# Performance work log

Measured on AMD Instinct MI355X. Metric: run time of the kernel, lower is better.

Reference implementation:

```python
import jax, jax.numpy as jnp
import numpy as np

R, N1, N2, D = 4, 4096, 4096, 8


def setup_inputs() -> dict:
    key = jax.random.key(0)
    k1, k2, k3 = jax.random.split(key, 3)
    x1 = jax.random.normal(k1, (R, N1, D), dtype=jnp.float32)
    x2 = jax.random.normal(k2, (R, N2, D), dtype=jnp.float32)
    # learned parameters (init: ones), matching nn.Parameter(torch.ones(...))
    lengthscales = jnp.ones((D, 1), dtype=jnp.float32)
    output_scale = jnp.ones((1,), dtype=jnp.float32)
    return {"x1": x1, "x2": x2, "lengthscales": lengthscales, "output_scale": output_scale}


def reference(x1, x2, lengthscales, output_scale):
    # RBF.K: output_scale^2 * exp(-0.5 * sum_d ((x1 - x2) / lengthscales)^2)
    # Computed via the Gram identity ||a-b||^2 = ||a||^2 + ||b||^2 - 2 a.b
    inv_ls = 1.0 / lengthscales.reshape(-1)          # [D]
    a = x1 * inv_ls                                  # [R, N1, D]
    b = x2 * inv_ls                                  # [R, N2, D]
    aa = jnp.sum(a * a, axis=-1)                     # [R, N1]
    bb = jnp.sum(b * b, axis=-1)                     # [R, N2]
    ab = jnp.einsum('rnd,rmd->rnm', a, b)            # [R, N1, N2]
    sqdist = jnp.maximum(aa[:, :, None] + bb[:, None, :] - 2.0 * ab, 0.0)
    return (output_scale[0] ** 2) * jnp.exp(-0.5 * sqdist)
```

## Files before the change

kernel.cpp:

```cpp
#include <hip/hip_runtime.h>


constexpr int D  = 8;
constexpr int BI = 16;
constexpr int BJ = 256;

#if __has_builtin(__builtin_amdgcn_exp2f)
#define FAST_EXP2(x) __builtin_amdgcn_exp2f(x)
#else
#define FAST_EXP2(x) __expf((x) * 0.69314718f)
#endif

__global__ __launch_bounds__(256, 6) void rbf_kernel(
    const float* __restrict__ x1, const float* __restrict__ x2,
    const float* __restrict__ ls, const float* __restrict__ osc,
    float* __restrict__ out, int N1, int N2)
{
    __shared__ float sb[D][BJ];
    __shared__ float sbb[BJ];
    __shared__ float sa[BI][D];
    __shared__ float sasq[BI];

    const int r   = blockIdx.z;
    const int i0  = blockIdx.y * BI;
    const int j0  = blockIdx.x * BJ;
    const int tid = threadIdx.x;

    float4 l0 = *reinterpret_cast<const float4*>(ls);
    float4 l1 = *reinterpret_cast<const float4*>(ls + 4);
    float4 inv0, inv1;
    inv0.x = 1.0f / l0.x; inv0.y = 1.0f / l0.y; inv0.z = 1.0f / l0.z; inv0.w = 1.0f / l0.w;
    inv1.x = 1.0f / l1.x; inv1.y = 1.0f / l1.y; inv1.z = 1.0f / l1.z; inv1.w = 1.0f / l1.w;

    {
        const float* src = x2 + ((size_t)r * N2 + j0 + tid) * D;
        float4 v0 = *reinterpret_cast<const float4*>(src);
        float4 v1 = *reinterpret_cast<const float4*>(src + 4);
        v0.x *= inv0.x; v0.y *= inv0.y; v0.z *= inv0.z; v0.w *= inv0.w;
        v1.x *= inv1.x; v1.y *= inv1.y; v1.z *= inv1.z; v1.w *= inv1.w;
        sb[0][tid] = v0.x; sb[1][tid] = v0.y; sb[2][tid] = v0.z; sb[3][tid] = v0.w;
        sb[4][tid] = v1.x; sb[5][tid] = v1.y; sb[6][tid] = v1.z; sb[7][tid] = v1.w;
        sbb[tid] = v0.x*v0.x + v0.y*v0.y + v0.z*v0.z + v0.w*v0.w
                 + v1.x*v1.x + v1.y*v1.y + v1.z*v1.z + v1.w*v1.w;
    }
    if (tid < BI) {
        const float* src = x1 + ((size_t)r * N1 + i0 + tid) * D;
        float4 v0 = *reinterpret_cast<const float4*>(src);
        float4 v1 = *reinterpret_cast<const float4*>(src + 4);
        v0.x *= inv0.x; v0.y *= inv0.y; v0.z *= inv0.z; v0.w *= inv0.w;
        v1.x *= inv1.x; v1.y *= inv1.y; v1.z *= inv1.z; v1.w *= inv1.w;
        *reinterpret_cast<float4*>(&sa[tid][0]) = v0;
        *reinterpret_cast<float4*>(&sa[tid][4]) = v1;
        sasq[tid] = v0.x*v0.x + v0.y*v0.y + v0.z*v0.z + v0.w*v0.w
                  + v1.x*v1.x + v1.y*v1.y + v1.z*v1.z + v1.w*v1.w;
    }
    const float os2 = osc[0] * osc[0];
    __syncthreads();

    const int lane = tid & 63;
    const int wv   = tid >> 6;

    float4 bd[D];
#pragma unroll
    for (int d = 0; d < D; ++d)
        bd[d] = *reinterpret_cast<const float4*>(&sb[d][lane * 4]);
    const float4 bb4 = *reinterpret_cast<const float4*>(&sbb[lane * 4]);

    constexpr float L2E  = 1.44269504f;
    constexpr float NH2E = -0.72134752f;

    float* obase = out + ((size_t)r * N1 + i0) * (size_t)N2 + j0 + lane * 4;

#pragma unroll
    for (int ii = 0; ii < 4; ++ii) {
        const int row = wv * 4 + ii;
        const float4 a0  = *reinterpret_cast<const float4*>(&sa[row][0]);
        const float4 a1  = *reinterpret_cast<const float4*>(&sa[row][4]);
        const float  asq = sasq[row];

        float4 ch;
        ch.x = (asq + bb4.x) * NH2E;
        ch.y = (asq + bb4.y) * NH2E;
        ch.z = (asq + bb4.z) * NH2E;
        ch.w = (asq + bb4.w) * NH2E;

        float d0 = 0.f, d1 = 0.f, d2 = 0.f, d3 = 0.f;
        const float a[D] = {a0.x, a0.y, a0.z, a0.w, a1.x, a1.y, a1.z, a1.w};
#pragma unroll
        for (int d = 0; d < D; ++d) {
            const float av = a[d];
            d0 = fmaf(av, bd[d].x, d0);
            d1 = fmaf(av, bd[d].y, d1);
            d2 = fmaf(av, bd[d].z, d2);
            d3 = fmaf(av, bd[d].w, d3);
        }
        float4 o;
        o.x = os2 * FAST_EXP2(fmaf(d0, L2E, ch.x));
        o.y = os2 * FAST_EXP2(fmaf(d1, L2E, ch.y));
        o.z = os2 * FAST_EXP2(fmaf(d2, L2E, ch.z));
        o.w = os2 * FAST_EXP2(fmaf(d3, L2E, ch.w));
        *reinterpret_cast<float4*>(obase + (size_t)row * N2) = o;
    }
}

extern "C" void kernel_launch(void* const* d_in, const int* in_sizes, int n_in,
                              void* d_out, int out_size, void* d_ws, size_t ws_size,
                              hipStream_t stream) {
    (void)in_sizes; (void)n_in; (void)d_ws; (void)ws_size; (void)out_size;
    const float* x1  = (const float*)d_in[0];
    const float* x2  = (const float*)d_in[1];
    const float* ls  = (const float*)d_in[2];
    const float* osc = (const float*)d_in[3];
    float* out = (float*)d_out;

    const int R = 4, N1 = 4096, N2 = 4096;
    dim3 grid(N2 / BJ, N1 / BI, R);
    rbf_kernel<<<grid, dim3(256), 0, stream>>>(x1, x2, ls, osc, out, N1, N2);
}
```

Baseline: 51.04 us.

## Enlarge row tile per block and fold output scale into exp argument

Each block now covers 128 rows of x1 instead of 16, with every wave looping over 32 rows and reusing its register-held x2 tile. This cuts the number of blocks and the repeated x2 loads and scaling setup per block. The output scale squared is folded into the exponent as log2, which removes a multiply per element. The occupancy hint is raised to 8. The log2 fold returns NaN or zero for a zero output scale, and the partial unroll of 4 may affect scheduling.

```diff
diff --git a/kernel.cpp b/kernel.cpp
--- a/kernel.cpp
+++ b/kernel.cpp
@@ -1,9 +1,9 @@
 #include <hip/hip_runtime.h>
 
 
-constexpr int D  = 8;
-constexpr int BI = 16;
-constexpr int BJ = 256;
+constexpr int D     = 8;
+constexpr int BROWS = 128;
+constexpr int BJ    = 256;
 
 #if __has_builtin(__builtin_amdgcn_exp2f)
 #define FAST_EXP2(x) __builtin_amdgcn_exp2f(x)
@@ -11,50 +11,55 @@
 #define FAST_EXP2(x) __expf((x) * 0.69314718f)
 #endif
 
-__global__ __launch_bounds__(256, 6) void rbf_kernel(
+__global__ __launch_bounds__(256, 8) void rbf_kernel(
     const float* __restrict__ x1, const float* __restrict__ x2,
     const float* __restrict__ ls, const float* __restrict__ osc,
     float* __restrict__ out, int N1, int N2)
 {
     __shared__ float sb[D][BJ];
     __shared__ float sbb[BJ];
-    __shared__ float sa[BI][D];
-    __shared__ float sasq[BI];
+    __shared__ float sa[BROWS][D];
+    __shared__ float sca[BROWS];
 
     const int r   = blockIdx.z;
-    const int i0  = blockIdx.y * BI;
+    const int i0  = blockIdx.y * BROWS;
     const int j0  = blockIdx.x * BJ;
     const int tid = threadIdx.x;
 
-    float4 l0 = *reinterpret_cast<const float4*>(ls);
-    float4 l1 = *reinterpret_cast<const float4*>(ls + 4);
-    float4 inv0, inv1;
-    inv0.x = 1.0f / l0.x; inv0.y = 1.0f / l0.y; inv0.z = 1.0f / l0.z; inv0.w = 1.0f / l0.w;
-    inv1.x = 1.0f / l1.x; inv1.y = 1.0f / l1.y; inv1.z = 1.0f / l1.z; inv1.w = 1.0f / l1.w;
+    constexpr float L2E  = 1.44269504f;
+    constexpr float NH2E = -0.72134752f;
 
     {
-        const float* src = x2 + ((size_t)r * N2 + j0 + tid) * D;
-        float4 v0 = *reinterpret_cast<const float4*>(src);
-        float4 v1 = *reinterpret_cast<const float4*>(src + 4);
-        v0.x *= inv0.x; v0.y *= inv0.y; v0.z *= inv0.z; v0.w *= inv0.w;
-        v1.x *= inv1.x; v1.y *= inv1.y; v1.z *= inv1.z; v1.w *= inv1.w;
-        sb[0][tid] = v0.x; sb[1][tid] = v0.y; sb[2][tid] = v0.z; sb[3][tid] = v0.w;
-        sb[4][tid] = v1.x; sb[5][tid] = v1.y; sb[6][tid] = v1.z; sb[7][tid] = v1.w;
-        sbb[tid] = v0.x*v0.x + v0.y*v0.y + v0.z*v0.z + v0.w*v0.w
-                 + v1.x*v1.x + v1.y*v1.y + v1.z*v1.z + v1.w*v1.w;
+        float4 l0 = *reinterpret_cast<const float4*>(ls);
+        float4 l1 = *reinterpret_cast<const float4*>(ls + 4);
+        float4 inv0, inv1;
+        inv0.x = 1.0f/l0.x; inv0.y = 1.0f/l0.y; inv0.z = 1.0f/l0.z; inv0.w = 1.0f/l0.w;
+        inv1.x = 1.0f/l1.x; inv1.y = 1.0f/l1.y; inv1.z = 1.0f/l1.z; inv1.w = 1.0f/l1.w;
+
+        {
+            const float* src = x2 + ((size_t)r * N2 + j0 + tid) * D;
+            float4 v0 = *reinterpret_cast<const float4*>(src);
+            float4 v1 = *reinterpret_cast<const float4*>(src + 4);
+            v0.x *= inv0.x; v0.y *= inv0.y; v0.z *= inv0.z; v0.w *= inv0.w;
+            v1.x *= inv1.x; v1.y *= inv1.y; v1.z *= inv1.z; v1.w *= inv1.w;
+            sb[0][tid] = v0.x; sb[1][tid] = v0.y; sb[2][tid] = v0.z; sb[3][tid] = v0.w;
+            sb[4][tid] = v1.x; sb[5][tid] = v1.y; sb[6][tid] = v1.z; sb[7][tid] = v1.w;
+            sbb[tid] = v0.x*v0.x + v0.y*v0.y + v0.z*v0.z + v0.w*v0.w
+                     + v1.x*v1.x + v1.y*v1.y + v1.z*v1.z + v1.w*v1.w;
+        }
+        if (tid < BROWS) {
+            const float* src = x1 + ((size_t)r * N1 + i0 + tid) * D;
+            float4 v0 = *reinterpret_cast<const float4*>(src);
+            float4 v1 = *reinterpret_cast<const float4*>(src + 4);
+            v0.x *= inv0.x; v0.y *= inv0.y; v0.z *= inv0.z; v0.w *= inv0.w;
+            v1.x *= inv1.x; v1.y *= inv1.y; v1.z *= inv1.z; v1.w *= inv1.w;
+            *reinterpret_cast<float4*>(&sa[tid][0]) = v0;
+            *reinterpret_cast<float4*>(&sa[tid][4]) = v1;
+            sca[tid] = (v0.x*v0.x + v0.y*v0.y + v0.z*v0.z + v0.w*v0.w
+                      + v1.x*v1.x + v1.y*v1.y + v1.z*v1.z + v1.w*v1.w) * NH2E;
+        }
     }
-    if (tid < BI) {
-        const float* src = x1 + ((size_t)r * N1 + i0 + tid) * D;
-        float4 v0 = *reinterpret_cast<const float4*>(src);
-        float4 v1 = *reinterpret_cast<const float4*>(src + 4);
-        v0.x *= inv0.x; v0.y *= inv0.y; v0.z *= inv0.z; v0.w *= inv0.w;
-        v1.x *= inv1.x; v1.y *= inv1.y; v1.z *= inv1.z; v1.w *= inv1.w;
-        *reinterpret_cast<float4*>(&sa[tid][0]) = v0;
-        *reinterpret_cast<float4*>(&sa[tid][4]) = v1;
-        sasq[tid] = v0.x*v0.x + v0.y*v0.y + v0.z*v0.z + v0.w*v0.w
-                  + v1.x*v1.x + v1.y*v1.y + v1.z*v1.z + v1.w*v1.w;
-    }
-    const float os2 = osc[0] * osc[0];
+    const float lg2os = __log2f(osc[0] * osc[0]);
     __syncthreads();
 
     const int lane = tid & 63;
@@ -64,42 +69,38 @@
 #pragma unroll
     for (int d = 0; d < D; ++d)
         bd[d] = *reinterpret_cast<const float4*>(&sb[d][lane * 4]);
-    const float4 bb4 = *reinterpret_cast<const float4*>(&sbb[lane * 4]);
+    float4 cb;
+    {
+        const float4 bb = *reinterpret_cast<const float4*>(&sbb[lane * 4]);
+        cb.x = fmaf(bb.x, NH2E, lg2os); cb.y = fmaf(bb.y, NH2E, lg2os);
+        cb.z = fmaf(bb.z, NH2E, lg2os); cb.w = fmaf(bb.w, NH2E, lg2os);
+    }
 
-    constexpr float L2E  = 1.44269504f;
-    constexpr float NH2E = -0.72134752f;
+    float* obase = out + ((size_t)r * N1 + i0 + wv * 32) * (size_t)N2 + j0 + lane * 4;
 
-    float* obase = out + ((size_t)r * N1 + i0) * (size_t)N2 + j0 + lane * 4;
+#pragma unroll 4
+    for (int ii = 0; ii < 32; ++ii) {
+        const int row = wv * 32 + ii;
+        const float4 a0 = *reinterpret_cast<const float4*>(&sa[row][0]);
+        const float4 a1 = *reinterpret_cast<const float4*>(&sa[row][4]);
+        const float  ca = sca[row];
 
-#pragma unroll
-    for (int ii = 0; ii < 4; ++ii) {
-        const int row = wv * 4 + ii;
-        const float4 a0  = *reinterpret_cast<const float4*>(&sa[row][0]);
-        const float4 a1  = *reinterpret_cast<const float4*>(&sa[row][4]);
-        const float  asq = sasq[row];
-
-        float4 ch;
-        ch.x = (asq + bb4.x) * NH2E;
-        ch.y = (asq + bb4.y) * NH2E;
-        ch.z = (asq + bb4.z) * NH2E;
-        ch.w = (asq + bb4.w) * NH2E;
-
-        float d0 = 0.f, d1 = 0.f, d2 = 0.f, d3 = 0.f;
+        float p0 = 0.f, p1 = 0.f, p2 = 0.f, p3 = 0.f;
         const float a[D] = {a0.x, a0.y, a0.z, a0.w, a1.x, a1.y, a1.z, a1.w};
 #pragma unroll
         for (int d = 0; d < D; ++d) {
             const float av = a[d];
-            d0 = fmaf(av, bd[d].x, d0);
-            d1 = fmaf(av, bd[d].y, d1);
-            d2 = fmaf(av, bd[d].z, d2);
-            d3 = fmaf(av, bd[d].w, d3);
+            p0 = fmaf(av, bd[d].x, p0);
+            p1 = fmaf(av, bd[d].y, p1);
+            p2 = fmaf(av, bd[d].z, p2);
+            p3 = fmaf(av, bd[d].w, p3);
         }
         float4 o;
-        o.x = os2 * FAST_EXP2(fmaf(d0, L2E, ch.x));
-        o.y = os2 * FAST_EXP2(fmaf(d1, L2E, ch.y));
-        o.z = os2 * FAST_EXP2(fmaf(d2, L2E, ch.z));
-        o.w = os2 * FAST_EXP2(fmaf(d3, L2E, ch.w));
-        *reinterpret_cast<float4*>(obase + (size_t)row * N2) = o;
+        o.x = FAST_EXP2(fmaf(p0, L2E, ca + cb.x));
+        o.y = FAST_EXP2(fmaf(p1, L2E, ca + cb.y));
+        o.z = FAST_EXP2(fmaf(p2, L2E, ca + cb.z));
+        o.w = FAST_EXP2(fmaf(p3, L2E, ca + cb.w));
+        *reinterpret_cast<float4*>(obase + (size_t)ii * N2) = o;
     }
 }
 
@@ -114,6 +115,6 @@
     float* out = (float*)d_out;
 
     const int R = 4, N1 = 4096, N2 = 4096;
-    dim3 grid(N2 / BJ, N1 / BI, R);
+    dim3 grid(N2 / BJ, N1 / BROWS, R);
     rbf_kernel<<<grid, dim3(256), 0, stream>>>(x1, x2, ls, osc, out, N1, N2);
 }
```

After: 55.83 us. +9.4%, slower.
